# Kernel optimization log

Measured on AMD Instinct MI355X. Metric: run time of the kernel, lower is better.

## Reference

```python
import jax, jax.numpy as jnp
import numpy as np

N = 50000      # nodes
E = 800000     # edges (avg degree 32 w/ 50k nodes -> 16 per direction here)
IN = 128       # in_channels
H = 64         # hidden_channels
G = 64         # graphs in the batch
C = 2          # num_classes


def setup_inputs() -> dict:
    key = jax.random.key(0)
    ks = jax.random.split(key, 8)
    x = jax.random.normal(ks[0], (N, IN), dtype=jnp.float32)
    edge_index = jax.random.randint(ks[1], (2, E), 0, N, dtype=jnp.int64)
    batch = jnp.sort(jax.random.randint(ks[2], (N,), 0, G, dtype=jnp.int64))
    # learned parameters (glorot-ish scale)
    W1 = jax.random.normal(ks[3], (IN, H), dtype=jnp.float32) * (1.0 / np.sqrt(IN))
    b1 = jnp.zeros((H,), dtype=jnp.float32)
    W2 = jax.random.normal(ks[4], (H, H), dtype=jnp.float32) * (1.0 / np.sqrt(H))
    b2 = jnp.zeros((H,), dtype=jnp.float32)
    Wl = jax.random.normal(ks[5], (H, C), dtype=jnp.float32) * (1.0 / np.sqrt(H))
    bl = jnp.zeros((C,), dtype=jnp.float32)
    return {"x": x, "edge_index": edge_index, "batch": batch,
            "W1": W1, "b1": b1, "W2": W2, "b2": b2, "Wl": Wl, "bl": bl}


def _gcn_conv(x, src, dst, W, b, n):
    # PyG GCNConv: linear transform, add self-loops, sym-normalize, scatter-add at dst
    h = x @ W                                   # [n, H]
    loop = jnp.arange(n, dtype=src.dtype)
    s = jnp.concatenate([src, loop])            # [E+n]
    d = jnp.concatenate([dst, loop])
    deg = jax.ops.segment_sum(jnp.ones_like(d, dtype=h.dtype), d, num_segments=n)
    dinv = deg ** -0.5                          # deg >= 1 due to self-loops
    norm = dinv[s] * dinv[d]                    # [E+n]
    msg = h[s] * norm[:, None]                  # gather + scale
    out = jax.ops.segment_sum(msg, d, num_segments=n)  # scatter-add aggregate
    return out + b


def reference(x, edge_index, batch, W1, b1, W2, b2, Wl, bl):
    src, dst = edge_index[0], edge_index[1]
    h = jax.nn.relu(_gcn_conv(x, src, dst, W1, b1, N))
    # dropout is identity in eval mode
    h = jax.nn.relu(_gcn_conv(h, src, dst, W2, b2, N))
    # global mean pool per graph
    counts = jax.ops.segment_sum(jnp.ones((N,), dtype=h.dtype), batch, num_segments=G)
    pooled = jax.ops.segment_sum(h, batch, num_segments=G) / jnp.maximum(counts, 1.0)[:, None]
    out = pooled @ Wl + bl                      # [G, C]
    return (out, pooled)
```

## Files before the change

kernel.cpp:

```cpp
#include <hip/hip_runtime.h>

#define N_NODES   50000
#define N_EDGES   800000
#define IN_CH     128
#define HID       64
#define N_GRAPHS  64
#define N_CLASSES 2
#define NBLK_SCAN ((N_NODES + 255) / 256)
#define NREP      32
#define FILL_CHUNKS ((N_EDGES + 2047) / 2048)
#define DEG_BLOCKS (FILL_CHUNKS * 8)


#define FMA4(xs, w, a) { (a).x = fmaf((xs), (w).x, (a).x); \
                         (a).y = fmaf((xs), (w).y, (a).y); \
                         (a).z = fmaf((xs), (w).z, (a).z); \
                         (a).w = fmaf((xs), (w).w, (a).w); }

__global__ __launch_bounds__(256) void deg_gemm1_kernel(const int* __restrict__ ei,
                                                        int* __restrict__ degCount,
                                                        const float* __restrict__ x,
                                                        const float* __restrict__ W1,
                                                        float* __restrict__ gg) {
    __shared__ float4 Ws[IN_CH * 16];
    if (blockIdx.x < DEG_BLOCKS) {
        int part = blockIdx.x & 7;
        int blk  = blockIdx.x >> 3;
        int lo   = part * 6250;
        int hi   = lo + 6250;
#pragma unroll
        for (int it = 0; it < 8; ++it) {
            int e = blk * 2048 + it * 256 + (int)threadIdx.x;
            if (e < N_EDGES) {
                int dst = ei[N_EDGES + e];
                if (dst >= lo && dst < hi) atomicAdd(&degCount[dst], 1);
            }
        }
        return;
    }
    int bid = blockIdx.x - DEG_BLOCKS;
    for (int i = threadIdx.x; i < IN_CH * 16; i += 256)
        Ws[i] = ((const float4*)W1)[i];
    __syncthreads();

    const int c4   = threadIdx.x & 15;
    const int rg   = threadIdx.x >> 4;
    const int row0 = bid * 128 + rg * 8;

    const float4* ap[8];
#pragma unroll
    for (int r = 0; r < 8; ++r) {
        int rowc = min(row0 + r, N_NODES - 1);
        ap[r] = (const float4*)(x + (size_t)rowc * IN_CH);
    }

    float4 acc[8] = {};
    for (int kk = 0; kk < IN_CH / 4; ++kk) {
        float4 xv[8];
#pragma unroll
        for (int r = 0; r < 8; ++r) xv[r] = ap[r][kk];
        float4 w;
        w = Ws[(4 * kk + 0) * 16 + c4];
#pragma unroll
        for (int r = 0; r < 8; ++r) FMA4(xv[r].x, w, acc[r]);
        w = Ws[(4 * kk + 1) * 16 + c4];
#pragma unroll
        for (int r = 0; r < 8; ++r) FMA4(xv[r].y, w, acc[r]);
        w = Ws[(4 * kk + 2) * 16 + c4];
#pragma unroll
        for (int r = 0; r < 8; ++r) FMA4(xv[r].z, w, acc[r]);
        w = Ws[(4 * kk + 3) * 16 + c4];
#pragma unroll
        for (int r = 0; r < 8; ++r) FMA4(xv[r].w, w, acc[r]);
    }

#pragma unroll
    for (int r = 0; r < 8; ++r) {
        int row = row0 + r;
        if (row < N_NODES)
            ((float4*)(gg + (size_t)row * HID))[c4] = acc[r];
    }
}

__global__ __launch_bounds__(256) void scan1_kernel(const int* __restrict__ degCount,
                                                    int* __restrict__ blockSums) {
    __shared__ int red[256];
    int i = blockIdx.x * 256 + threadIdx.x;
    red[threadIdx.x] = (i < N_NODES) ? degCount[i] : 0;
    __syncthreads();
    for (int off = 128; off > 0; off >>= 1) {
        if (threadIdx.x < off) red[threadIdx.x] += red[threadIdx.x + off];
        __syncthreads();
    }
    if (threadIdx.x == 0) blockSums[blockIdx.x] = red[0];
}

__global__ __launch_bounds__(256) void scan2_kernel(int* __restrict__ blockSums) {
    __shared__ int s[256];
    int t = threadIdx.x;
    int v = (t < NBLK_SCAN) ? blockSums[t] : 0;
    s[t] = v;
    __syncthreads();
    for (int off = 1; off < 256; off <<= 1) {
        int a = (t >= off) ? s[t - off] : 0;
        __syncthreads();
        s[t] += a;
        __syncthreads();
    }
    if (t < NBLK_SCAN) blockSums[t] = s[t] - v;
}

__global__ __launch_bounds__(256) void scan3_kernel(int* __restrict__ degFill,
                                                    const int* __restrict__ blockSums,
                                                    int* __restrict__ rowPtr,
                                                    float* __restrict__ dinv) {
    __shared__ int s[256];
    int t = threadIdx.x;
    int i = blockIdx.x * 256 + t;
    int d = (i < N_NODES) ? degFill[i] : 0;
    s[t] = d;
    __syncthreads();
    for (int off = 1; off < 256; off <<= 1) {
        int a = (t >= off) ? s[t - off] : 0;
        __syncthreads();
        s[t] += a;
        __syncthreads();
    }
    int excl = s[t] - d + blockSums[blockIdx.x];
    if (i < N_NODES) {
        rowPtr[i]  = excl;
        degFill[i] = excl;
        dinv[i]    = 1.0f / sqrtf((float)(d + 1));
    }
    if (i == 0) rowPtr[N_NODES] = N_EDGES;
}

__global__ __launch_bounds__(256) void fill_kernel(const int* __restrict__ ei,
                                                   int* __restrict__ fillPtr,
                                                   int* __restrict__ colIdx) {
    int part = blockIdx.x & 7;
    int blk  = blockIdx.x >> 3;
    int lo   = part * 6250;
    int hi   = lo + 6250;
#pragma unroll
    for (int it = 0; it < 8; ++it) {
        int e = blk * 2048 + it * 256 + (int)threadIdx.x;
        if (e < N_EDGES) {
            int dst = ei[N_EDGES + e];
            if (dst >= lo && dst < hi) {
                int src = ei[e];
                int pos = atomicAdd(&fillPtr[dst], 1);
                colIdx[pos] = src;
            }
        }
    }
}

template <int K>
__global__ __launch_bounds__(256) void gemm_kernel(const float* __restrict__ A,
                                                   const float* __restrict__ W,
                                                   const float* __restrict__ dinv,
                                                   float* __restrict__ out) {
    __shared__ float4 Ws[K * 16];
    for (int i = threadIdx.x; i < K * 16; i += 256)
        Ws[i] = ((const float4*)W)[i];
    __syncthreads();

    const int c4   = threadIdx.x & 15;
    const int rg   = threadIdx.x >> 4;
    const int row0 = blockIdx.x * 128 + rg * 8;

    const float4* ap[8];
#pragma unroll
    for (int r = 0; r < 8; ++r) {
        int rowc = min(row0 + r, N_NODES - 1);
        ap[r] = (const float4*)(A + (size_t)rowc * K);
    }

    float4 acc[8] = {};
    for (int kk = 0; kk < K / 4; ++kk) {
        float4 xv[8];
#pragma unroll
        for (int r = 0; r < 8; ++r) xv[r] = ap[r][kk];
        float4 w;
        w = Ws[(4 * kk + 0) * 16 + c4];
#pragma unroll
        for (int r = 0; r < 8; ++r) FMA4(xv[r].x, w, acc[r]);
        w = Ws[(4 * kk + 1) * 16 + c4];
#pragma unroll
        for (int r = 0; r < 8; ++r) FMA4(xv[r].y, w, acc[r]);
        w = Ws[(4 * kk + 2) * 16 + c4];
#pragma unroll
        for (int r = 0; r < 8; ++r) FMA4(xv[r].z, w, acc[r]);
        w = Ws[(4 * kk + 3) * 16 + c4];
#pragma unroll
        for (int r = 0; r < 8; ++r) FMA4(xv[r].w, w, acc[r]);
    }

#pragma unroll
    for (int r = 0; r < 8; ++r) {
        int row = row0 + r;
        if (row < N_NODES) {
            float dv = dinv[row];
            float4 o = acc[r];
            o.x *= dv; o.y *= dv; o.z *= dv; o.w *= dv;
            ((float4*)(out + (size_t)row * HID))[c4] = o;
        }
    }
}

__global__ __launch_bounds__(256) void agg1_kernel(const float* __restrict__ gg,
                                                   const float* __restrict__ dinv,
                                                   const int* __restrict__ rowPtr,
                                                   const int* __restrict__ colIdx,
                                                   const float* __restrict__ bias,
                                                   float* __restrict__ out) {
    int lane = threadIdx.x & 63;
    int v = blockIdx.x * 4 + (threadIdx.x >> 6);
    if (v >= N_NODES) return;

    const float dv = dinv[v];
    float accA = dv * gg[(size_t)v * HID + lane];
    float accB = 0.f;
    int e0 = rowPtr[v];
    int e1 = rowPtr[v + 1];
    for (int e = e0; e < e1; e += 8) {
        int   u[8];
        float du[8];
#pragma unroll
        for (int i = 0; i < 8; ++i) {
            int idx = min(e + i, e1 - 1);
            u[i]  = colIdx[idx];
            du[i] = (e + i < e1) ? dinv[u[i]] : 0.f;
        }
#pragma unroll
        for (int i = 0; i < 8; ++i) {
            float a = gg[(size_t)u[i] * HID + lane];
            if (i & 1) accB = fmaf(du[i], a, accB);
            else       accA = fmaf(du[i], a, accA);
        }
    }
    float r = dv * (accA + accB) + bias[lane];
    out[(size_t)v * HID + lane] = fmaxf(r, 0.f);
}

__global__ __launch_bounds__(256) void agg2pool_kernel(const float* __restrict__ g,
                                                       const float* __restrict__ dinv,
                                                       const int* __restrict__ rowPtr,
                                                       const int* __restrict__ colIdx,
                                                       const float* __restrict__ bias,
                                                       const int* __restrict__ batch,
                                                       float* __restrict__ pooledSum) {
    int lane = threadIdx.x & 63;
    int v = blockIdx.x * 4 + (threadIdx.x >> 6);
    if (v >= N_NODES) return;

    float accA = g[(size_t)v * HID + lane];
    float accB = 0.f;
    int e0 = rowPtr[v];
    int e1 = rowPtr[v + 1];
    for (int e = e0; e < e1; e += 8) {
        int   u[8];
        float wsel[8];
#pragma unroll
        for (int i = 0; i < 8; ++i) {
            int idx = min(e + i, e1 - 1);
            u[i]    = colIdx[idx];
            wsel[i] = (e + i < e1) ? 1.f : 0.f;
        }
#pragma unroll
        for (int i = 0; i < 8; ++i) {
            float a = g[(size_t)u[i] * HID + lane];
            if (i & 1) accB = fmaf(wsel[i], a, accB);
            else       accA = fmaf(wsel[i], a, accA);
        }
    }
    float r = fmaxf(dinv[v] * (accA + accB) + bias[lane], 0.f);
    int gid = batch[v];
    int rep = blockIdx.x & (NREP - 1);
    atomicAdd(&pooledSum[(size_t)rep * N_GRAPHS * HID + gid * HID + lane], r);
}

__global__ __launch_bounds__(64) void pool2_kernel(const float* __restrict__ pooledSum,
                                                   const int* __restrict__ batch,
                                                   const float* __restrict__ Wl,
                                                   const float* __restrict__ bl,
                                                   float* __restrict__ dout) {
    int g    = blockIdx.x;
    int lane = threadIdx.x;

    int lo0 = 0, hi = N_NODES;
    while (lo0 < hi) { int mid = (lo0 + hi) >> 1; if (batch[mid] < g) lo0 = mid + 1; else hi = mid; }
    int lo1 = lo0; hi = N_NODES;
    while (lo1 < hi) { int mid = (lo1 + hi) >> 1; if (batch[mid] < g + 1) lo1 = mid + 1; else hi = mid; }
    float cnt = (float)(lo1 - lo0);

    float s = 0.f;
#pragma unroll
    for (int rep = 0; rep < NREP; ++rep)
        s += pooledSum[(size_t)rep * N_GRAPHS * HID + g * HID + lane];

    float p = s / fmaxf(cnt, 1.0f);
    dout[N_GRAPHS * N_CLASSES + g * HID + lane] = p;

    float p0 = p * Wl[lane * N_CLASSES + 0];
    float p1 = p * Wl[lane * N_CLASSES + 1];
#pragma unroll
    for (int off = 32; off > 0; off >>= 1) {
        p0 += __shfl_down(p0, off, 64);
        p1 += __shfl_down(p1, off, 64);
    }
    if (lane == 0) {
        dout[g * N_CLASSES + 0] = p0 + bl[0];
        dout[g * N_CLASSES + 1] = p1 + bl[1];
    }
}

extern "C" void kernel_launch(void* const* d_in, const int* in_sizes, int n_in,
                              void* d_out, int out_size, void* d_ws, size_t ws_size,
                              hipStream_t stream) {
    const float* x     = (const float*)d_in[0];
    const int*   ei    = (const int*)d_in[1];
    const int*   batch = (const int*)d_in[2];
    const float* W1    = (const float*)d_in[3];
    const float* b1    = (const float*)d_in[4];
    const float* W2    = (const float*)d_in[5];
    const float* b2    = (const float*)d_in[6];
    const float* Wl    = (const float*)d_in[7];
    const float* bl    = (const float*)d_in[8];
    float* out = (float*)d_out;

    char* ws = (char*)d_ws;
    size_t off = 0;
    auto alloc = [&](size_t bytes) -> void* {
        void* p = ws + off;
        off += (bytes + 255) & ~(size_t)255;
        return p;
    };
    int*   degFill   = (int*)  alloc((size_t)N_NODES * 4);
    int*   rowPtr    = (int*)  alloc((size_t)(N_NODES + 1) * 4);
    float* dinv      = (float*)alloc((size_t)N_NODES * 4);
    int*   blockSums = (int*)  alloc((size_t)NBLK_SCAN * 4);
    float* pooledSum = (float*)alloc((size_t)NREP * N_GRAPHS * HID * 4);
    int*   colIdx    = (int*)  alloc((size_t)N_EDGES * 4);
    float* bufA      = (float*)alloc((size_t)N_NODES * HID * 4);
    float* bufB      = (float*)alloc((size_t)N_NODES * HID * 4);

    hipMemsetAsync(degFill, 0, (size_t)N_NODES * 4, stream);
    hipMemsetAsync(pooledSum, 0, (size_t)NREP * N_GRAPHS * HID * 4, stream);

    deg_gemm1_kernel<<<DEG_BLOCKS + (N_NODES + 127) / 128, 256, 0, stream>>>(
        ei, degFill, x, W1, bufA);
    scan1_kernel<<<NBLK_SCAN, 256, 0, stream>>>(degFill, blockSums);
    scan2_kernel<<<1, 256, 0, stream>>>(blockSums);
    scan3_kernel<<<NBLK_SCAN, 256, 0, stream>>>(degFill, blockSums, rowPtr, dinv);
    fill_kernel <<<DEG_BLOCKS, 256, 0, stream>>>(ei, degFill, colIdx);

    agg1_kernel<<<N_NODES / 4, 256, 0, stream>>>(bufA, dinv, rowPtr, colIdx, b1, bufB);

    gemm_kernel<HID><<<(N_NODES + 127) / 128, 256, 0, stream>>>(bufB, W2, dinv, bufA);
    agg2pool_kernel <<<N_NODES / 4, 256, 0, stream>>>(bufA, dinv, rowPtr, colIdx, b2, batch, pooledSum);

    pool2_kernel<<<N_GRAPHS, 64, 0, stream>>>(pooledSum, batch, Wl, bl, out);
}
```

Before: 320.3 us.

## Move GEMM1 into fill kernel with dinv prescale; split wave per edge pair in aggregation

GEMM1 moves out of the degree kernel and into the CSR fill kernel, interleaved one GEMM block per nine blocks. Its output is now prescaled by dinv, so agg1 no longer gathers dinv[u] for every edge. Both aggregation kernels now have each half-wave handle alternate edges with float2 loads, 16 edges per iteration, and combine the halves with a cross-half shuffle. The aim is fewer dependent per-edge loads and more memory parallelism in the gather. The cost is that GEMM1 reads W1 from global memory instead of shared memory, and the interleaved block index mapping is complex.

Measured after the change: 289.2 us. 9.7% less time.

```diff
diff --git a/kernel.cpp b/kernel.cpp
--- a/kernel.cpp
+++ b/kernel.cpp
@@ -10,75 +10,22 @@
 #define NREP      32
 #define FILL_CHUNKS ((N_EDGES + 2047) / 2048)
 #define DEG_BLOCKS (FILL_CHUNKS * 8)
-
-
-#define FMA4(xs, w, a) { (a).x = fmaf((xs), (w).x, (a).x); \
-                         (a).y = fmaf((xs), (w).y, (a).y); \
-                         (a).z = fmaf((xs), (w).z, (a).z); \
-                         (a).w = fmaf((xs), (w).w, (a).w); }
-
-__global__ __launch_bounds__(256) void deg_gemm1_kernel(const int* __restrict__ ei,
-                                                        int* __restrict__ degCount,
-                                                        const float* __restrict__ x,
-                                                        const float* __restrict__ W1,
-                                                        float* __restrict__ gg) {
-    __shared__ float4 Ws[IN_CH * 16];
-    if (blockIdx.x < DEG_BLOCKS) {
-        int part = blockIdx.x & 7;
-        int blk  = blockIdx.x >> 3;
-        int lo   = part * 6250;
-        int hi   = lo + 6250;
-#pragma unroll
-        for (int it = 0; it < 8; ++it) {
-            int e = blk * 2048 + it * 256 + (int)threadIdx.x;
-            if (e < N_EDGES) {
-                int dst = ei[N_EDGES + e];
-                if (dst >= lo && dst < hi) atomicAdd(&degCount[dst], 1);
-            }
-        }
-        return;
-    }
-    int bid = blockIdx.x - DEG_BLOCKS;
-    for (int i = threadIdx.x; i < IN_CH * 16; i += 256)
-        Ws[i] = ((const float4*)W1)[i];
-    __syncthreads();
-
-    const int c4   = threadIdx.x & 15;
-    const int rg   = threadIdx.x >> 4;
-    const int row0 = bid * 128 + rg * 8;
-
-    const float4* ap[8];
-#pragma unroll
-    for (int r = 0; r < 8; ++r) {
-        int rowc = min(row0 + r, N_NODES - 1);
-        ap[r] = (const float4*)(x + (size_t)rowc * IN_CH);
-    }
-
-    float4 acc[8] = {};
-    for (int kk = 0; kk < IN_CH / 4; ++kk) {
-        float4 xv[8];
-#pragma unroll
-        for (int r = 0; r < 8; ++r) xv[r] = ap[r][kk];
-        float4 w;
-        w = Ws[(4 * kk + 0) * 16 + c4];
-#pragma unroll
-        for (int r = 0; r < 8; ++r) FMA4(xv[r].x, w, acc[r]);
-        w = Ws[(4 * kk + 1) * 16 + c4];
-#pragma unroll
-        for (int r = 0; r < 8; ++r) FMA4(xv[r].y, w, acc[r]);
-        w = Ws[(4 * kk + 2) * 16 + c4];
-#pragma unroll
-        for (int r = 0; r < 8; ++r) FMA4(xv[r].z, w, acc[r]);
-        w = Ws[(4 * kk + 3) * 16 + c4];
-#pragma unroll
-        for (int r = 0; r < 8; ++r) FMA4(xv[r].w, w, acc[r]);
-    }
-
-#pragma unroll
-    for (int r = 0; r < 8; ++r) {
-        int row = row0 + r;
-        if (row < N_NODES)
-            ((float4*)(gg + (size_t)row * HID))[c4] = acc[r];
+#define GEMM1_BLOCKS ((N_NODES + 127) / 128)
+
+
+__global__ __launch_bounds__(256) void deg_kernel(const int* __restrict__ ei,
+                                                  int* __restrict__ degCount) {
+    int part = blockIdx.x & 7;
+    int blk  = blockIdx.x >> 3;
+    int lo   = part * 6250;
+    int hi   = lo + 6250;
+#pragma unroll
+    for (int it = 0; it < 8; ++it) {
+        int e = blk * 2048 + it * 256 + (int)threadIdx.x;
+        if (e < N_EDGES) {
+            int dst = ei[N_EDGES + e];
+            if (dst >= lo && dst < hi) atomicAdd(&degCount[dst], 1);
+        }
     }
 }
 
@@ -135,11 +82,68 @@
     if (i == 0) rowPtr[N_NODES] = N_EDGES;
 }
 
-__global__ __launch_bounds__(256) void fill_kernel(const int* __restrict__ ei,
-                                                   int* __restrict__ fillPtr,
-                                                   int* __restrict__ colIdx) {
-    int part = blockIdx.x & 7;
-    int blk  = blockIdx.x >> 3;
+#define FMA4(xs, w, a) { (a).x = fmaf((xs), (w).x, (a).x); \
+                         (a).y = fmaf((xs), (w).y, (a).y); \
+                         (a).z = fmaf((xs), (w).z, (a).z); \
+                         (a).w = fmaf((xs), (w).w, (a).w); }
+
+__global__ __launch_bounds__(256) void fill_gemm1_kernel(const int* __restrict__ ei,
+                                                         int* __restrict__ fillPtr,
+                                                         int* __restrict__ colIdx,
+                                                         const float* __restrict__ x,
+                                                         const float* __restrict__ W1,
+                                                         const float* __restrict__ dinv,
+                                                         float* __restrict__ out) {
+    int div9 = blockIdx.x / 9;
+    if ((blockIdx.x % 9) == 0 && div9 < GEMM1_BLOCKS) {
+        const float4* W4 = (const float4*)W1;
+        const int c4   = threadIdx.x & 15;
+        const int rg   = threadIdx.x >> 4;
+        const int row0 = div9 * 128 + rg * 8;
+
+        const float4* ap[8];
+#pragma unroll
+        for (int r = 0; r < 8; ++r) {
+            int rowc = min(row0 + r, N_NODES - 1);
+            ap[r] = (const float4*)(x + (size_t)rowc * IN_CH);
+        }
+
+        float4 acc[8] = {};
+        for (int kk = 0; kk < IN_CH / 4; ++kk) {
+            float4 xv[8];
+#pragma unroll
+            for (int r = 0; r < 8; ++r) xv[r] = ap[r][kk];
+            float4 w;
+            w = W4[(4 * kk + 0) * 16 + c4];
+#pragma unroll
+            for (int r = 0; r < 8; ++r) FMA4(xv[r].x, w, acc[r]);
+            w = W4[(4 * kk + 1) * 16 + c4];
+#pragma unroll
+            for (int r = 0; r < 8; ++r) FMA4(xv[r].y, w, acc[r]);
+            w = W4[(4 * kk + 2) * 16 + c4];
+#pragma unroll
+            for (int r = 0; r < 8; ++r) FMA4(xv[r].z, w, acc[r]);
+            w = W4[(4 * kk + 3) * 16 + c4];
+#pragma unroll
+            for (int r = 0; r < 8; ++r) FMA4(xv[r].w, w, acc[r]);
+        }
+
+#pragma unroll
+        for (int r = 0; r < 8; ++r) {
+            int row = row0 + r;
+            if (row < N_NODES) {
+                float dv = dinv[row];
+                float4 o = acc[r];
+                o.x *= dv; o.y *= dv; o.z *= dv; o.w *= dv;
+                ((float4*)(out + (size_t)row * HID))[c4] = o;
+            }
+        }
+        return;
+    }
+    int fill_bid = blockIdx.x - div9 - ((blockIdx.x % 9) ? 1 : 0);
+    if ((blockIdx.x % 9) == 0) fill_bid = blockIdx.x - div9;
+    int part = fill_bid & 7;
+    int blk  = fill_bid >> 3;
     int lo   = part * 6250;
     int hi   = lo + 6250;
 #pragma unroll
@@ -209,39 +213,50 @@
     }
 }
 
-__global__ __launch_bounds__(256) void agg1_kernel(const float* __restrict__ gg,
+__global__ __launch_bounds__(256) void agg1_kernel(const float* __restrict__ g,
                                                    const float* __restrict__ dinv,
                                                    const int* __restrict__ rowPtr,
                                                    const int* __restrict__ colIdx,
                                                    const float* __restrict__ bias,
                                                    float* __restrict__ out) {
     int lane = threadIdx.x & 63;
+    int half = lane >> 5;
+    int hl   = lane & 31;
     int v = blockIdx.x * 4 + (threadIdx.x >> 6);
     if (v >= N_NODES) return;
 
-    const float dv = dinv[v];
-    float accA = dv * gg[(size_t)v * HID + lane];
-    float accB = 0.f;
+    const float2* g2 = (const float2*)g;
+    float2 acc = {0.f, 0.f};
+    if (half == 0) acc = g2[(size_t)v * 32 + hl];
+
     int e0 = rowPtr[v];
     int e1 = rowPtr[v + 1];
-    for (int e = e0; e < e1; e += 8) {
+    for (int e = e0; e < e1; e += 16) {
         int   u[8];
-        float du[8];
-#pragma unroll
-        for (int i = 0; i < 8; ++i) {
-            int idx = min(e + i, e1 - 1);
-            u[i]  = colIdx[idx];
-            du[i] = (e + i < e1) ? dinv[u[i]] : 0.f;
-        }
-#pragma unroll
-        for (int i = 0; i < 8; ++i) {
-            float a = gg[(size_t)u[i] * HID + lane];
-            if (i & 1) accB = fmaf(du[i], a, accB);
-            else       accA = fmaf(du[i], a, accA);
-        }
-    }
-    float r = dv * (accA + accB) + bias[lane];
-    out[(size_t)v * HID + lane] = fmaxf(r, 0.f);
+        float wsel[8];
+#pragma unroll
+        for (int k = 0; k < 8; ++k) {
+            int ee  = e + 2 * k + half;
+            int idx = min(ee, e1 - 1);
+            u[k]    = colIdx[idx];
+            wsel[k] = (ee < e1) ? 1.f : 0.f;
+        }
+#pragma unroll
+        for (int k = 0; k < 8; ++k) {
+            float2 a = g2[(size_t)u[k] * 32 + hl];
+            acc.x = fmaf(wsel[k], a.x, acc.x);
+            acc.y = fmaf(wsel[k], a.y, acc.y);
+        }
+    }
+    acc.x += __shfl_xor(acc.x, 32);
+    acc.y += __shfl_xor(acc.y, 32);
+
+    float dv = dinv[v];
+    float2 b = ((const float2*)bias)[hl];
+    float2 r;
+    r.x = fmaxf(dv * acc.x + b.x, 0.f);
+    r.y = fmaxf(dv * acc.y + b.y, 0.f);
+    if (half == 0) ((float2*)(out + (size_t)v * HID))[hl] = r;
 }
 
 __global__ __launch_bounds__(256) void agg2pool_kernel(const float* __restrict__ g,
@@ -252,33 +267,46 @@
                                                        const int* __restrict__ batch,
                                                        float* __restrict__ pooledSum) {
     int lane = threadIdx.x & 63;
+    int half = lane >> 5;
+    int hl   = lane & 31;
     int v = blockIdx.x * 4 + (threadIdx.x >> 6);
     if (v >= N_NODES) return;
 
-    float accA = g[(size_t)v * HID + lane];
-    float accB = 0.f;
+    const float2* g2 = (const float2*)g;
+    float2 acc = {0.f, 0.f};
+    if (half == 0) acc = g2[(size_t)v * 32 + hl];
+
     int e0 = rowPtr[v];
     int e1 = rowPtr[v + 1];
-    for (int e = e0; e < e1; e += 8) {
+    for (int e = e0; e < e1; e += 16) {
         int   u[8];
         float wsel[8];
 #pragma unroll
-        for (int i = 0; i < 8; ++i) {
-            int idx = min(e + i, e1 - 1);
-            u[i]    = colIdx[idx];
-            wsel[i] = (e + i < e1) ? 1.f : 0.f;
-        }
-#pragma unroll
-        for (int i = 0; i < 8; ++i) {
-            float a = g[(size_t)u[i] * HID + lane];
-            if (i & 1) accB = fmaf(wsel[i], a, accB);
-            else       accA = fmaf(wsel[i], a, accA);
-        }
-    }
-    float r = fmaxf(dinv[v] * (accA + accB) + bias[lane], 0.f);
+        for (int k = 0; k < 8; ++k) {
+            int ee  = e + 2 * k + half;
+            int idx = min(ee, e1 - 1);
+            u[k]    = colIdx[idx];
+            wsel[k] = (ee < e1) ? 1.f : 0.f;
+        }
+#pragma unroll
+        for (int k = 0; k < 8; ++k) {
+            float2 a = g2[(size_t)u[k] * 32 + hl];
+            acc.x = fmaf(wsel[k], a.x, acc.x);
+            acc.y = fmaf(wsel[k], a.y, acc.y);
+        }
+    }
+    acc.x += __shfl_xor(acc.x, 32);
+    acc.y += __shfl_xor(acc.y, 32);
+
+    float dv = dinv[v];
+    float2 b = ((const float2*)bias)[hl];
+    float rx = fmaxf(dv * acc.x + b.x, 0.f);
+    float ry = fmaxf(dv * acc.y + b.y, 0.f);
+
     int gid = batch[v];
     int rep = blockIdx.x & (NREP - 1);
-    atomicAdd(&pooledSum[(size_t)rep * N_GRAPHS * HID + gid * HID + lane], r);
+    atomicAdd(&pooledSum[(size_t)rep * N_GRAPHS * HID + gid * HID + 2 * hl + half],
+              half ? ry : rx);
 }
 
 __global__ __launch_bounds__(64) void pool2_kernel(const float* __restrict__ pooledSum,
@@ -349,16 +377,17 @@
     hipMemsetAsync(degFill, 0, (size_t)N_NODES * 4, stream);
     hipMemsetAsync(pooledSum, 0, (size_t)NREP * N_GRAPHS * HID * 4, stream);
 
-    deg_gemm1_kernel<<<DEG_BLOCKS + (N_NODES + 127) / 128, 256, 0, stream>>>(
-        ei, degFill, x, W1, bufA);
+    deg_kernel  <<<DEG_BLOCKS, 256, 0, stream>>>(ei, degFill);
     scan1_kernel<<<NBLK_SCAN, 256, 0, stream>>>(degFill, blockSums);
     scan2_kernel<<<1, 256, 0, stream>>>(blockSums);
     scan3_kernel<<<NBLK_SCAN, 256, 0, stream>>>(degFill, blockSums, rowPtr, dinv);
-    fill_kernel <<<DEG_BLOCKS, 256, 0, stream>>>(ei, degFill, colIdx);
+
+    fill_gemm1_kernel<<<DEG_BLOCKS + GEMM1_BLOCKS, 256, 0, stream>>>(
+        ei, degFill, colIdx, x, W1, dinv, bufA);
 
     agg1_kernel<<<N_NODES / 4, 256, 0, stream>>>(bufA, dinv, rowPtr, colIdx, b1, bufB);
 
-    gemm_kernel<HID><<<(N_NODES + 127) / 128, 256, 0, stream>>>(bufB, W2, dinv, bufA);
+    gemm_kernel<HID><<<GEMM1_BLOCKS, 256, 0, stream>>>(bufB, W2, dinv, bufA);
     agg2pool_kernel <<<N_NODES / 4, 256, 0, stream>>>(bufA, dinv, rowPtr, colIdx, b2, batch, pooledSum);
 
     pool2_kernel<<<N_GRAPHS, 64, 0, stream>>>(pooledSum, batch, Wl, bl, out);
```
